# Optimization experiments

Hardware: AMD Instinct MI355X
Metric: run time of the kernel (lower is better)

Reference implementation:

```python
import jax, jax.numpy as jnp
import numpy as np

B, H, C_LEN, Q_LEN = 64, 128, 1024, 128


def setup_inputs() -> dict:
    key = jax.random.key(0)
    k1, k2, k3 = jax.random.split(key, 3)
    context = jax.random.normal(k1, (B, H, C_LEN), dtype=jnp.float32)
    question = jax.random.normal(k2, (B, H, Q_LEN), dtype=jnp.float32)
    lim = np.sqrt(1.0 / H)
    w = jax.random.uniform(k3, (3 * H,), dtype=jnp.float32, minval=-lim, maxval=lim)
    return {"context": context, "question": question, "w": w}


def reference(context, question, w):
    # context: (B, H, C), question: (B, H, Q); w: (3H,) with cat order (q, c, cq)
    h = w.shape[0] // 3
    w_q, w_c, w_cq = w[:h], w[h:2 * h], w[2 * h:]
    c = jnp.transpose(context, (0, 2, 1))   # (B, C, H)
    q = jnp.transpose(question, (0, 2, 1))  # (B, Q, H)
    # trilinear similarity s[b,i,j] = c_i.w_c + q_j.w_q + (c_i*w_cq).q_j  -> (B, C, Q)
    s = (c @ w_c)[:, :, None] + (q @ w_q)[:, None, :] \
        + jnp.einsum('bih,bjh->bij', c * w_cq, q)
    # original applies softmax over dim=1 (context axis) for BOTH s1 and s2
    s1 = jax.nn.softmax(s, axis=1)           # (B, C, Q)
    a = jnp.einsum('bij,bjh->bih', s1, q)    # (B, C, H)
    l = jnp.einsum('bij,bkj->bik', s1, s1)   # (B, C, C)
    b = jnp.einsum('bik,bkh->bih', l, c)     # (B, C, H)
    out = jnp.concatenate([c, a, c * a, c * b], axis=2)  # (B, C, 4H)
    # dropout disabled (drop_prob=0) for deterministic reference
    return jnp.transpose(out, (0, 2, 1))     # (B, 4H, C)
```

## Files before the change

kernel.cpp:

```cpp
#include <hip/hip_runtime.h>

#define BB 64
#define HH 128
#define CC 1024
#define QQ 128

typedef unsigned short u16;
typedef unsigned int u32;
using bf16x8 = __attribute__((ext_vector_type(8))) short;
using f32x4 = __attribute__((ext_vector_type(4))) float;

#define MFMA16(a, b, c) __builtin_amdgcn_mfma_f32_16x16x32_bf16(a, b, c, 0, 0, 0)

__device__ __forceinline__ u16 f2b(float f) {
  union { float f; u32 i; } v; v.f = f;
  u32 r = v.i + 0x7FFFu + ((v.i >> 16) & 1u);
  return (u16)(r >> 16);
}
__device__ __forceinline__ u32 pack_hi2(float a, float b) {
  return (__float_as_uint(a) >> 16) | (__float_as_uint(b) & 0xFFFF0000u);
}
__device__ __forceinline__ u32 pack_lo2(float a, float b) {
  float ra = a - __uint_as_float(__float_as_uint(a) & 0xFFFF0000u);
  float rb = b - __uint_as_float(__float_as_uint(b) & 0xFFFF0000u);
  return (__float_as_uint(ra) >> 16) | (__float_as_uint(rb) & 0xFFFF0000u);
}

__device__ __forceinline__ void stage16(const float* __restrict__ p,
                                        u16* dhi, u16* dlo) {
  float4 a0 = *(const float4*)p;
  float4 a1 = *(const float4*)(p + 4);
  float4 a2 = *(const float4*)(p + 8);
  float4 a3 = *(const float4*)(p + 12);
  uint4 h0 = {pack_hi2(a0.x, a0.y), pack_hi2(a0.z, a0.w),
              pack_hi2(a1.x, a1.y), pack_hi2(a1.z, a1.w)};
  uint4 h1 = {pack_hi2(a2.x, a2.y), pack_hi2(a2.z, a2.w),
              pack_hi2(a3.x, a3.y), pack_hi2(a3.z, a3.w)};
  uint4 l0 = {pack_lo2(a0.x, a0.y), pack_lo2(a0.z, a0.w),
              pack_lo2(a1.x, a1.y), pack_lo2(a1.z, a1.w)};
  uint4 l1 = {pack_lo2(a2.x, a2.y), pack_lo2(a2.z, a2.w),
              pack_lo2(a3.x, a3.y), pack_lo2(a3.z, a3.w)};
  *(uint4*)dhi = h0;
  *(uint4*)(dhi + 8) = h1;
  *(uint4*)dlo = l0;
  *(uint4*)(dlo + 8) = l1;
}

__global__ __launch_bounds__(256) void k_qw(
    const float* __restrict__ qst, const float* __restrict__ w,
    u16* __restrict__ qwh, u16* __restrict__ qwl) {
  const int b = blockIdx.x;
  const int tid = threadIdx.x;
  __shared__ float ld[128 * 129];
  __shared__ float wcq[128];
  const float* qb = qst + (size_t)b * HH * QQ;
#pragma unroll
  for (int rep = 0; rep < 16; ++rep) {
    int h = rep * 8 + (tid >> 5);
    int jo = (tid & 31) * 4;
    float4 v = *(const float4*)(qb + (size_t)h * QQ + jo);
    float* d = &ld[h * 129 + jo];
    d[0] = v.x; d[1] = v.y; d[2] = v.z; d[3] = v.w;
  }
  if (tid < 128) wcq[tid] = w[2 * HH + tid];
  __syncthreads();
  const int j = tid >> 1;
  const int hh0 = (tid & 1) * 64;
  u16* oh = qwh + (size_t)b * 144 * 128 + j * 128 + hh0;
  u16* ol = qwl + (size_t)b * 144 * 128 + j * 128 + hh0;
#pragma unroll
  for (int g = 0; g < 8; ++g) {
    u32 hw[4], lw[4];
#pragma unroll
    for (int p = 0; p < 4; ++p) {
      int h = hh0 + g * 8 + p * 2;
      float a = ld[h * 129 + j] * wcq[h];
      float c = ld[(h + 1) * 129 + j] * wcq[h + 1];
      hw[p] = pack_hi2(a, c);
      lw[p] = pack_lo2(a, c);
    }
    uint4 vh = {hw[0], hw[1], hw[2], hw[3]};
    uint4 vl = {lw[0], lw[1], lw[2], lw[3]};
    *(uint4*)(oh + g * 8) = vh;
    *(uint4*)(ol + g * 8) = vl;
  }
  if (tid < 128) {
    int jr = 128 + (tid >> 3);
    int hc = (tid & 7) * 16;
    u32 hw[8], lw[8];
#pragma unroll
    for (int p = 0; p < 8; ++p) { hw[p] = 0; lw[p] = 0; }
    if (jr == 128) {
#pragma unroll
      for (int p = 0; p < 8; ++p) {
        float a = w[HH + hc + p * 2];
        float c = w[HH + hc + p * 2 + 1];
        hw[p] = pack_hi2(a, c);
        lw[p] = pack_lo2(a, c);
      }
    }
    u16* ph = qwh + (size_t)b * 144 * 128 + (size_t)jr * 128 + hc;
    u16* pl = qwl + (size_t)b * 144 * 128 + (size_t)jr * 128 + hc;
    uint4 vh0 = {hw[0], hw[1], hw[2], hw[3]};
    uint4 vh1 = {hw[4], hw[5], hw[6], hw[7]};
    uint4 vl0 = {lw[0], lw[1], lw[2], lw[3]};
    uint4 vl1 = {lw[4], lw[5], lw[6], lw[7]};
    *(uint4*)ph = vh0; *(uint4*)(ph + 8) = vh1;
    *(uint4*)pl = vl0; *(uint4*)(pl + 8) = vl1;
  }
}

__global__ __launch_bounds__(256) void k_ct(
    const float* __restrict__ ctx, u16* __restrict__ cTh) {
  const int b = blockIdx.x;
  const int i0 = blockIdx.y * 128;
  const int tid = threadIdx.x;
  __shared__ float ld[128 * 129];
  const float* cb = ctx + (size_t)b * HH * CC;
#pragma unroll
  for (int rep = 0; rep < 16; ++rep) {
    int h = rep * 8 + (tid >> 5);
    int io = (tid & 31) * 4;
    float4 v = *(const float4*)(cb + (size_t)h * CC + i0 + io);
    float* d = &ld[h * 129 + io];
    d[0] = v.x; d[1] = v.y; d[2] = v.z; d[3] = v.w;
  }
  __syncthreads();
  const int i = tid >> 1;
  const int hh0 = (tid & 1) * 64;
  u16* oh = cTh + (size_t)b * CC * HH + (size_t)(i0 + i) * 128 + hh0;
#pragma unroll
  for (int g = 0; g < 8; ++g) {
    u32 hw[4];
#pragma unroll
    for (int p = 0; p < 4; ++p) {
      int h = hh0 + g * 8 + p * 2;
      hw[p] = pack_hi2(ld[h * 129 + i], ld[(h + 1) * 129 + i]);
    }
    uint4 vh = {hw[0], hw[1], hw[2], hw[3]};
    *(uint4*)(oh + g * 8) = vh;
  }
}

__global__ __launch_bounds__(512) void k0_softmax(
    const u16* __restrict__ cTh, const u16* __restrict__ qwh,
    const u16* __restrict__ qwl, u16* __restrict__ s1ws,
    u16* __restrict__ s1tb) {
  const int b = blockIdx.x;
  const int j0 = blockIdx.y * 16;
  const int tid = threadIdx.x;
  const int lane = tid & 63;
  const int wv = tid >> 6;
  const int l15 = lane & 15, l4 = lane >> 4;
  __shared__ float wred[2][8][4][4];

  const u16* cb = cTh + (size_t)b * CC * HH;
  const u16* qhp = qwh + (size_t)b * 144 * 128;
  const u16* qlp = qwl + (size_t)b * 144 * 128;

  bf16x8 aqh[4], aql[4], axh[4];
#pragma unroll
  for (int kk = 0; kk < 4; ++kk) {
    const int off = kk * 32 + l4 * 8;
    aqh[kk] = *(const bf16x8*)(qhp + (size_t)(j0 + l15) * 128 + off);
    aql[kk] = *(const bf16x8*)(qlp + (size_t)(j0 + l15) * 128 + off);
    axh[kk] = *(const bf16x8*)(qhp + (size_t)(128 + l15) * 128 + off);
  }

  f32x4 sv[8];
  float cwcv[8];
#pragma unroll
  for (int it = 0; it < 8; ++it) {
    const int i = wv * 128 + it * 16 + l15;
    f32x4 aR = {0.f, 0.f, 0.f, 0.f};
    f32x4 aX = {0.f, 0.f, 0.f, 0.f};
#pragma unroll
    for (int kk = 0; kk < 4; ++kk) {
      bf16x8 bh = *(const bf16x8*)(cb + (size_t)i * 128 + kk * 32 + l4 * 8);
      aR = MFMA16(aqh[kk], bh, aR);
      aR = MFMA16(aql[kk], bh, aR);
      aX = MFMA16(axh[kk], bh, aX);
    }
    cwcv[it] = __shfl(aX[0], l15);
    sv[it] = aR;
  }
#pragma unroll
  for (int it = 0; it < 8; ++it)
#pragma unroll
    for (int r = 0; r < 4; ++r) sv[it][r] += cwcv[it];

  float mj[4];
#pragma unroll
  for (int r = 0; r < 4; ++r) {
    float m = sv[0][r];
#pragma unroll
    for (int it = 1; it < 8; ++it) m = fmaxf(m, sv[it][r]);
#pragma unroll
    for (int msk = 1; msk < 16; msk <<= 1) m = fmaxf(m, __shfl_xor(m, msk));
    mj[r] = m;
  }
  if (l15 == 0) {
#pragma unroll
    for (int r = 0; r < 4; ++r) wred[0][wv][l4][r] = mj[r];
  }
  __syncthreads();
  float gm[4];
#pragma unroll
  for (int r = 0; r < 4; ++r) {
    float m = wred[0][0][l4][r];
#pragma unroll
    for (int w2 = 1; w2 < 8; ++w2) m = fmaxf(m, wred[0][w2][l4][r]);
    gm[r] = m;
  }

#pragma unroll
  for (int it = 0; it < 8; ++it)
#pragma unroll
    for (int r = 0; r < 4; ++r) sv[it][r] = __expf(sv[it][r] - gm[r]);
  float sj[4];
#pragma unroll
  for (int r = 0; r < 4; ++r) {
    float s = 0.f;
#pragma unroll
    for (int it = 0; it < 8; ++it) s += sv[it][r];
#pragma unroll
    for (int msk = 1; msk < 16; msk <<= 1) s += __shfl_xor(s, msk);
    sj[r] = s;
  }
  if (l15 == 0) {
#pragma unroll
    for (int r = 0; r < 4; ++r) wred[1][wv][l4][r] = sj[r];
  }
  __syncthreads();
  float inv_[4];
#pragma unroll
  for (int r = 0; r < 4; ++r) {
    float s = 0.f;
#pragma unroll
    for (int w2 = 0; w2 < 8; ++w2) s += wred[1][w2][l4][r];
    inv_[r] = 1.0f / s;
  }

  u16* ws = s1ws + (size_t)b * QQ * CC;
  u16* tb = s1tb + (size_t)b * (16 * 1024 * 8);
#pragma unroll
  for (int it = 0; it < 8; ++it) {
    const int i = wv * 128 + it * 16 + l15;
#pragma unroll
    for (int r = 0; r < 4; ++r) {
      const int j = j0 + l4 * 4 + r;
      u16 pv = f2b(sv[it][r] * inv_[r]);
      ws[(size_t)j * CC + i] = pv;
      tb[((size_t)(j >> 3) * 1024 + i) * 8 + (j & 7)] = pv;
    }
  }
}

__global__ __launch_bounds__(256) void k2_t(
    const float* __restrict__ ctx, const u16* __restrict__ s1ws,
    float* __restrict__ tT) {
  const int b = blockIdx.x;
  const int h0 = (blockIdx.y >> 1) * 32;
  const int j0 = (blockIdx.y & 1) * 64;
  const int tid = threadIdx.x;
  const int lane = tid & 63;
  const int wv = tid >> 6;
  const int l15 = lane & 15, l4 = lane >> 4;

  __shared__ u16 sHi[32 * 136];
  __shared__ u16 sLo[32 * 136];

  f32x4 acc[2];
  acc[0] = 0.f; acc[1] = 0.f;

  const float* cb = ctx + ((size_t)b * HH + h0) * CC;
  const u16* sb = s1ws + ((size_t)b * QQ + j0 + wv * 16 + l15) * CC;
  const int srow = tid >> 3;
  const int scol = (tid & 7) * 16;

  for (int k0 = 0; k0 < CC; k0 += 128) {
    __syncthreads();
    stage16(cb + (size_t)srow * CC + k0 + scol,
            &sHi[srow * 136 + scol], &sLo[srow * 136 + scol]);
    __syncthreads();
#pragma unroll
    for (int kk = 0; kk < 4; ++kk) {
      bf16x8 bf = *(const bf16x8*)(sb + k0 + kk * 32 + l4 * 8);
#pragma unroll
      for (int ht = 0; ht < 2; ++ht) {
        const int ar = (ht * 16 + l15) * 136 + kk * 32 + l4 * 8;
        bf16x8 ah = *(const bf16x8*)&sHi[ar];
        bf16x8 al = *(const bf16x8*)&sLo[ar];
        acc[ht] = MFMA16(ah, bf, acc[ht]);
        acc[ht] = MFMA16(al, bf, acc[ht]);
      }
    }
  }
  float* tb = tT + (size_t)b * HH * QQ;
#pragma unroll
  for (int ht = 0; ht < 2; ++ht)
#pragma unroll
    for (int r = 0; r < 4; ++r)
      tb[(size_t)(h0 + ht * 16 + l4 * 4 + r) * QQ + j0 + wv * 16 + l15] =
          acc[ht][r];
}

__global__ __launch_bounds__(256, 2) void k3_out(
    const float* __restrict__ ctx, const float* __restrict__ qst,
    const u16* __restrict__ s1tb, const float* __restrict__ tT,
    float* __restrict__ out) {
  const int b = blockIdx.x;
  const int i0 = blockIdx.y * 128;
  const int tid = threadIdx.x;
  const int lane = tid & 63;
  const int wv = tid >> 6;
  const int l15 = lane & 15, l4 = lane >> 4;

  __shared__ u16 qHi[128 * 40], qLo[128 * 40];
  __shared__ u16 tHi[128 * 40], tLo[128 * 40];

  f32x4 accA[8][2], accB[8][2];
#pragma unroll
  for (int it = 0; it < 8; ++it)
#pragma unroll
    for (int ht = 0; ht < 2; ++ht) { accA[it][ht] = 0.f; accB[it][ht] = 0.f; }

  const u16* stb = s1tb + (size_t)b * (16 * 1024 * 8);
  const float* qb = qst + (size_t)b * HH * QQ;
  const float* tb = tT + (size_t)b * HH * QQ;
  const int srow = tid >> 1;
  const int scol = (tid & 1) * 16;

  for (int ks = 0; ks < 4; ++ks) {
    const int jb = ks * 32;
    __syncthreads();
    stage16(qb + (size_t)srow * QQ + jb + scol,
            &qHi[srow * 40 + scol], &qLo[srow * 40 + scol]);
    stage16(tb + (size_t)srow * QQ + jb + scol,
            &tHi[srow * 40 + scol], &tLo[srow * 40 + scol]);
    __syncthreads();
    bf16x8 qh[2], ql[2], th[2], tl[2];
#pragma unroll
    for (int ht = 0; ht < 2; ++ht) {
      const int ar = (wv * 32 + ht * 16 + l15) * 40 + l4 * 8;
      qh[ht] = *(const bf16x8*)&qHi[ar];
      ql[ht] = *(const bf16x8*)&qLo[ar];
      th[ht] = *(const bf16x8*)&tHi[ar];
      tl[ht] = *(const bf16x8*)&tLo[ar];
    }
#pragma unroll
    for (int half = 0; half < 2; ++half) {
      bf16x8 bfr[4];
#pragma unroll
      for (int t4 = 0; t4 < 4; ++t4) {
        const int it = half * 4 + t4;
        bfr[t4] = *(const bf16x8*)(stb +
            ((size_t)(ks * 4 + l4) * 1024 + i0 + it * 16 + l15) * 8);
      }
#pragma unroll
      for (int t4 = 0; t4 < 4; ++t4) {
        const int it = half * 4 + t4;
#pragma unroll
        for (int ht = 0; ht < 2; ++ht) {
          accA[it][ht] = MFMA16(qh[ht], bfr[t4], accA[it][ht]);
          accA[it][ht] = MFMA16(ql[ht], bfr[t4], accA[it][ht]);
          accB[it][ht] = MFMA16(th[ht], bfr[t4], accB[it][ht]);
          accB[it][ht] = MFMA16(tl[ht], bfr[t4], accB[it][ht]);
        }
      }
    }
  }

  const float* cb = ctx + (size_t)b * HH * CC;
  float* ob = out + (size_t)b * 4 * HH * CC;
#pragma unroll
  for (int it = 0; it < 8; ++it) {
    const int ii = i0 + it * 16 + l15;
#pragma unroll
    for (int ht = 0; ht < 2; ++ht) {
#pragma unroll
      for (int r = 0; r < 4; ++r) {
        const int h = wv * 32 + ht * 16 + l4 * 4 + r;
        const size_t base = (size_t)h * CC + ii;
        const float cv = cb[base];
        const float av = accA[it][ht][r];
        const float bv = accB[it][ht][r];
        ob[base] = cv;
        ob[(size_t)HH * CC + base] = av;
        ob[(size_t)2 * HH * CC + base] = cv * av;
        ob[(size_t)3 * HH * CC + base] = cv * bv;
      }
    }
  }
}

extern "C" void kernel_launch(void* const* d_in, const int* in_sizes, int n_in,
                              void* d_out, int out_size, void* d_ws, size_t ws_size,
                              hipStream_t stream) {
  const float* ctx = (const float*)d_in[0];
  const float* qst = (const float*)d_in[1];
  const float* w = (const float*)d_in[2];
  for (int k = 0; k < n_in; ++k) {
    if (in_sizes[k] == BB * HH * CC) ctx = (const float*)d_in[k];
    else if (in_sizes[k] == BB * HH * QQ) qst = (const float*)d_in[k];
    else if (in_sizes[k] == 3 * HH) w = (const float*)d_in[k];
  }
  float* out = (float*)d_out;

  u16* s1ws = (u16*)d_ws;
  u16* s1tb = (u16*)((char*)d_ws + (size_t)16 * 1024 * 1024);
  float* tT = (float*)((char*)d_ws + (size_t)32 * 1024 * 1024);

  char* ob = (char*)d_out;
  u16* qwl = (u16*)(ob + 112721920);
  u16* qwh = (u16*)(ob + 115081216);
  u16* cTh = (u16*)(ob + 117440512);

  k_qw<<<BB, 256, 0, stream>>>(qst, w, qwh, qwl);
  k_ct<<<dim3(BB, 8), 256, 0, stream>>>(ctx, cTh);
  k0_softmax<<<dim3(BB, 8), 512, 0, stream>>>(cTh, qwh, qwl, s1ws, s1tb);
  k2_t<<<dim3(BB, 8), 256, 0, stream>>>(ctx, s1ws, tT);
  k3_out<<<dim3(BB, 8), 256, 0, stream>>>(ctx, qst, s1tb, tT, out);
}
```

Before: 245.7 us.

## Fuse prep kernels and fold context-by-softmax product into softmax kernel

Merges the question-weight and context-transpose prep kernels into one launch with an extra grid row. Folds the k2_t reduction (context times s1 over the context axis) into the softmax kernel: the normalized s1 tile is kept in LDS and each wave reads the context rows straight from global memory, splitting them into hi/lo bf16 for MFMA. This removes the s1ws global round-trip and two launches. In exchange, every softmax block now re-reads the full per-batch context (8x redundant across j-blocks), and there is a larger LDS footprint.

Result: no change. 248.9 us, median of 2 (+1.3%).

```diff
diff --git a/kernel.cpp b/kernel.cpp
--- a/kernel.cpp
+++ b/kernel.cpp
@@ -46,106 +46,105 @@
   *(uint4*)(dlo + 8) = l1;
 }
 
-__global__ __launch_bounds__(256) void k_qw(
-    const float* __restrict__ qst, const float* __restrict__ w,
+__global__ __launch_bounds__(256) void k_prep(
+    const float* __restrict__ ctx, const float* __restrict__ qst,
+    const float* __restrict__ w, u16* __restrict__ cTh,
     u16* __restrict__ qwh, u16* __restrict__ qwl) {
   const int b = blockIdx.x;
+  const int y = blockIdx.y;
   const int tid = threadIdx.x;
   __shared__ float ld[128 * 129];
   __shared__ float wcq[128];
-  const float* qb = qst + (size_t)b * HH * QQ;
-#pragma unroll
-  for (int rep = 0; rep < 16; ++rep) {
-    int h = rep * 8 + (tid >> 5);
-    int jo = (tid & 31) * 4;
-    float4 v = *(const float4*)(qb + (size_t)h * QQ + jo);
-    float* d = &ld[h * 129 + jo];
-    d[0] = v.x; d[1] = v.y; d[2] = v.z; d[3] = v.w;
-  }
-  if (tid < 128) wcq[tid] = w[2 * HH + tid];
-  __syncthreads();
-  const int j = tid >> 1;
-  const int hh0 = (tid & 1) * 64;
-  u16* oh = qwh + (size_t)b * 144 * 128 + j * 128 + hh0;
-  u16* ol = qwl + (size_t)b * 144 * 128 + j * 128 + hh0;
-#pragma unroll
-  for (int g = 0; g < 8; ++g) {
-    u32 hw[4], lw[4];
-#pragma unroll
-    for (int p = 0; p < 4; ++p) {
-      int h = hh0 + g * 8 + p * 2;
-      float a = ld[h * 129 + j] * wcq[h];
-      float c = ld[(h + 1) * 129 + j] * wcq[h + 1];
-      hw[p] = pack_hi2(a, c);
-      lw[p] = pack_lo2(a, c);
-    }
-    uint4 vh = {hw[0], hw[1], hw[2], hw[3]};
-    uint4 vl = {lw[0], lw[1], lw[2], lw[3]};
-    *(uint4*)(oh + g * 8) = vh;
-    *(uint4*)(ol + g * 8) = vl;
-  }
-  if (tid < 128) {
-    int jr = 128 + (tid >> 3);
-    int hc = (tid & 7) * 16;
-    u32 hw[8], lw[8];
-#pragma unroll
-    for (int p = 0; p < 8; ++p) { hw[p] = 0; lw[p] = 0; }
-    if (jr == 128) {
-#pragma unroll
-      for (int p = 0; p < 8; ++p) {
-        float a = w[HH + hc + p * 2];
-        float c = w[HH + hc + p * 2 + 1];
+
+  if (y < 8) {
+    const int i0 = y * 128;
+    const float* cb = ctx + (size_t)b * HH * CC;
+#pragma unroll
+    for (int rep = 0; rep < 16; ++rep) {
+      int h = rep * 8 + (tid >> 5);
+      int io = (tid & 31) * 4;
+      float4 v = *(const float4*)(cb + (size_t)h * CC + i0 + io);
+      float* d = &ld[h * 129 + io];
+      d[0] = v.x; d[1] = v.y; d[2] = v.z; d[3] = v.w;
+    }
+    __syncthreads();
+    const int i = tid >> 1;
+    const int hh0 = (tid & 1) * 64;
+    u16* oh = cTh + (size_t)b * CC * HH + (size_t)(i0 + i) * 128 + hh0;
+#pragma unroll
+    for (int g = 0; g < 8; ++g) {
+      u32 hw[4];
+#pragma unroll
+      for (int p = 0; p < 4; ++p) {
+        int h = hh0 + g * 8 + p * 2;
+        hw[p] = pack_hi2(ld[h * 129 + i], ld[(h + 1) * 129 + i]);
+      }
+      uint4 vh = {hw[0], hw[1], hw[2], hw[3]};
+      *(uint4*)(oh + g * 8) = vh;
+    }
+  } else {
+    const float* qb = qst + (size_t)b * HH * QQ;
+#pragma unroll
+    for (int rep = 0; rep < 16; ++rep) {
+      int h = rep * 8 + (tid >> 5);
+      int jo = (tid & 31) * 4;
+      float4 v = *(const float4*)(qb + (size_t)h * QQ + jo);
+      float* d = &ld[h * 129 + jo];
+      d[0] = v.x; d[1] = v.y; d[2] = v.z; d[3] = v.w;
+    }
+    if (tid < 128) wcq[tid] = w[2 * HH + tid];
+    __syncthreads();
+    const int j = tid >> 1;
+    const int hh0 = (tid & 1) * 64;
+    u16* oh = qwh + (size_t)b * 144 * 128 + j * 128 + hh0;
+    u16* ol = qwl + (size_t)b * 144 * 128 + j * 128 + hh0;
+#pragma unroll
+    for (int g = 0; g < 8; ++g) {
+      u32 hw[4], lw[4];
+#pragma unroll
+      for (int p = 0; p < 4; ++p) {
+        int h = hh0 + g * 8 + p * 2;
+        float a = ld[h * 129 + j] * wcq[h];
+        float c = ld[(h + 1) * 129 + j] * wcq[h + 1];
         hw[p] = pack_hi2(a, c);
         lw[p] = pack_lo2(a, c);
       }
-    }
-    u16* ph = qwh + (size_t)b * 144 * 128 + (size_t)jr * 128 + hc;
-    u16* pl = qwl + (size_t)b * 144 * 128 + (size_t)jr * 128 + hc;
-    uint4 vh0 = {hw[0], hw[1], hw[2], hw[3]};
-    uint4 vh1 = {hw[4], hw[5], hw[6], hw[7]};
-    uint4 vl0 = {lw[0], lw[1], lw[2], lw[3]};
-    uint4 vl1 = {lw[4], lw[5], lw[6], lw[7]};
-    *(uint4*)ph = vh0; *(uint4*)(ph + 8) = vh1;
-    *(uint4*)pl = vl0; *(uint4*)(pl + 8) = vl1;
-  }
-}
-
-__global__ __launch_bounds__(256) void k_ct(
-    const float* __restrict__ ctx, u16* __restrict__ cTh) {
-  const int b = blockIdx.x;
-  const int i0 = blockIdx.y * 128;
-  const int tid = threadIdx.x;
-  __shared__ float ld[128 * 129];
-  const float* cb = ctx + (size_t)b * HH * CC;
-#pragma unroll
-  for (int rep = 0; rep < 16; ++rep) {
-    int h = rep * 8 + (tid >> 5);
-    int io = (tid & 31) * 4;
-    float4 v = *(const float4*)(cb + (size_t)h * CC + i0 + io);
-    float* d = &ld[h * 129 + io];
-    d[0] = v.x; d[1] = v.y; d[2] = v.z; d[3] = v.w;
-  }
-  __syncthreads();
-  const int i = tid >> 1;
-  const int hh0 = (tid & 1) * 64;
-  u16* oh = cTh + (size_t)b * CC * HH + (size_t)(i0 + i) * 128 + hh0;
-#pragma unroll
-  for (int g = 0; g < 8; ++g) {
-    u32 hw[4];
-#pragma unroll
-    for (int p = 0; p < 4; ++p) {
-      int h = hh0 + g * 8 + p * 2;
-      hw[p] = pack_hi2(ld[h * 129 + i], ld[(h + 1) * 129 + i]);
-    }
-    uint4 vh = {hw[0], hw[1], hw[2], hw[3]};
-    *(uint4*)(oh + g * 8) = vh;
-  }
-}
-
-__global__ __launch_bounds__(512) void k0_softmax(
-    const u16* __restrict__ cTh, const u16* __restrict__ qwh,
-    const u16* __restrict__ qwl, u16* __restrict__ s1ws,
-    u16* __restrict__ s1tb) {
+      uint4 vh = {hw[0], hw[1], hw[2], hw[3]};
+      uint4 vl = {lw[0], lw[1], lw[2], lw[3]};
+      *(uint4*)(oh + g * 8) = vh;
+      *(uint4*)(ol + g * 8) = vl;
+    }
+    if (tid < 128) {
+      int jr = 128 + (tid >> 3);
+      int hc = (tid & 7) * 16;
+      u32 hw[8], lw[8];
+#pragma unroll
+      for (int p = 0; p < 8; ++p) { hw[p] = 0; lw[p] = 0; }
+      if (jr == 128) {
+#pragma unroll
+        for (int p = 0; p < 8; ++p) {
+          float a = w[HH + hc + p * 2];
+          float c = w[HH + hc + p * 2 + 1];
+          hw[p] = pack_hi2(a, c);
+          lw[p] = pack_lo2(a, c);
+        }
+      }
+      u16* ph = qwh + (size_t)b * 144 * 128 + (size_t)jr * 128 + hc;
+      u16* pl = qwl + (size_t)b * 144 * 128 + (size_t)jr * 128 + hc;
+      uint4 vh0 = {hw[0], hw[1], hw[2], hw[3]};
+      uint4 vh1 = {hw[4], hw[5], hw[6], hw[7]};
+      uint4 vl0 = {lw[0], lw[1], lw[2], lw[3]};
+      uint4 vl1 = {lw[4], lw[5], lw[6], lw[7]};
+      *(uint4*)ph = vh0; *(uint4*)(ph + 8) = vh1;
+      *(uint4*)pl = vl0; *(uint4*)(pl + 8) = vl1;
+    }
+  }
+}
+
+__global__ __launch_bounds__(512) void k0_fused(
+    const float* __restrict__ ctx, const u16* __restrict__ cTh,
+    const u16* __restrict__ qwh, const u16* __restrict__ qwl,
+    u16* __restrict__ s1tb, float* __restrict__ tT) {
   const int b = blockIdx.x;
   const int j0 = blockIdx.y * 16;
   const int tid = threadIdx.x;
@@ -153,6 +152,7 @@
   const int wv = tid >> 6;
   const int l15 = lane & 15, l4 = lane >> 4;
   __shared__ float wred[2][8][4][4];
+  __shared__ u16 s1l[16 * 1026];
 
   const u16* cb = cTh + (size_t)b * CC * HH;
   const u16* qhp = qwh + (size_t)b * 144 * 128;
@@ -241,7 +241,6 @@
     inv_[r] = 1.0f / s;
   }
 
-  u16* ws = s1ws + (size_t)b * QQ * CC;
   u16* tb = s1tb + (size_t)b * (16 * 1024 * 8);
 #pragma unroll
   for (int it = 0; it < 8; ++it) {
@@ -250,59 +249,30 @@
     for (int r = 0; r < 4; ++r) {
       const int j = j0 + l4 * 4 + r;
       u16 pv = f2b(sv[it][r] * inv_[r]);
-      ws[(size_t)j * CC + i] = pv;
       tb[((size_t)(j >> 3) * 1024 + i) * 8 + (j & 7)] = pv;
-    }
-  }
-}
-
-__global__ __launch_bounds__(256) void k2_t(
-    const float* __restrict__ ctx, const u16* __restrict__ s1ws,
-    float* __restrict__ tT) {
-  const int b = blockIdx.x;
-  const int h0 = (blockIdx.y >> 1) * 32;
-  const int j0 = (blockIdx.y & 1) * 64;
-  const int tid = threadIdx.x;
-  const int lane = tid & 63;
-  const int wv = tid >> 6;
-  const int l15 = lane & 15, l4 = lane >> 4;
-
-  __shared__ u16 sHi[32 * 136];
-  __shared__ u16 sLo[32 * 136];
-
-  f32x4 acc[2];
-  acc[0] = 0.f; acc[1] = 0.f;
-
-  const float* cb = ctx + ((size_t)b * HH + h0) * CC;
-  const u16* sb = s1ws + ((size_t)b * QQ + j0 + wv * 16 + l15) * CC;
-  const int srow = tid >> 3;
-  const int scol = (tid & 7) * 16;
-
-  for (int k0 = 0; k0 < CC; k0 += 128) {
-    __syncthreads();
-    stage16(cb + (size_t)srow * CC + k0 + scol,
-            &sHi[srow * 136 + scol], &sLo[srow * 136 + scol]);
-    __syncthreads();
-#pragma unroll
-    for (int kk = 0; kk < 4; ++kk) {
-      bf16x8 bf = *(const bf16x8*)(sb + k0 + kk * 32 + l4 * 8);
-#pragma unroll
-      for (int ht = 0; ht < 2; ++ht) {
-        const int ar = (ht * 16 + l15) * 136 + kk * 32 + l4 * 8;
-        bf16x8 ah = *(const bf16x8*)&sHi[ar];
-        bf16x8 al = *(const bf16x8*)&sLo[ar];
-        acc[ht] = MFMA16(ah, bf, acc[ht]);
-        acc[ht] = MFMA16(al, bf, acc[ht]);
-      }
-    }
-  }
-  float* tb = tT + (size_t)b * HH * QQ;
-#pragma unroll
-  for (int ht = 0; ht < 2; ++ht)
-#pragma unroll
-    for (int r = 0; r < 4; ++r)
-      tb[(size_t)(h0 + ht * 16 + l4 * 4 + r) * QQ + j0 + wv * 16 + l15] =
-          acc[ht][r];
+      s1l[(l4 * 4 + r) * 1026 + i] = pv;
+    }
+  }
+  __syncthreads();
+
+  const float* cxr = ctx + ((size_t)b * HH + wv * 16 + l15) * CC;
+  f32x4 tacc = {0.f, 0.f, 0.f, 0.f};
+#pragma unroll 4
+  for (int kk = 0; kk < 32; ++kk) {
+    const int ib = kk * 32 + l4 * 8;
+    float4 c0 = *(const float4*)(cxr + ib);
+    float4 c1 = *(const float4*)(cxr + ib + 4);
+    uint4 hb = {pack_hi2(c0.x, c0.y), pack_hi2(c0.z, c0.w),
+                pack_hi2(c1.x, c1.y), pack_hi2(c1.z, c1.w)};
+    uint4 lb = {pack_lo2(c0.x, c0.y), pack_lo2(c0.z, c0.w),
+                pack_lo2(c1.x, c1.y), pack_lo2(c1.z, c1.w)};
+    bf16x8 af = *(const bf16x8*)&s1l[l15 * 1026 + ib];
+    tacc = MFMA16(af, *(const bf16x8*)&hb, tacc);
+    tacc = MFMA16(af, *(const bf16x8*)&lb, tacc);
+  }
+  float* tw = tT + (size_t)b * HH * QQ + (size_t)(wv * 16 + l15) * QQ + j0;
+#pragma unroll
+  for (int r = 0; r < 4; ++r) tw[l4 * 4 + r] = tacc[r];
 }
 
 __global__ __launch_bounds__(256, 2) void k3_out(
@@ -407,18 +377,15 @@
   }
   float* out = (float*)d_out;
 
-  u16* s1ws = (u16*)d_ws;
-  u16* s1tb = (u16*)((char*)d_ws + (size_t)16 * 1024 * 1024);
-  float* tT = (float*)((char*)d_ws + (size_t)32 * 1024 * 1024);
+  u16* s1tb = (u16*)d_ws;
+  float* tT = (float*)((char*)d_ws + (size_t)16 * 1024 * 1024);
 
   char* ob = (char*)d_out;
   u16* qwl = (u16*)(ob + 112721920);
   u16* qwh = (u16*)(ob + 115081216);
   u16* cTh = (u16*)(ob + 117440512);
 
-  k_qw<<<BB, 256, 0, stream>>>(qst, w, qwh, qwl);
-  k_ct<<<dim3(BB, 8), 256, 0, stream>>>(ctx, cTh);
-  k0_softmax<<<dim3(BB, 8), 512, 0, stream>>>(cTh, qwh, qwl, s1ws, s1tb);
-  k2_t<<<dim3(BB, 8), 256, 0, stream>>>(ctx, s1ws, tT);
+  k_prep<<<dim3(BB, 9), 256, 0, stream>>>(ctx, qst, w, cTh, qwh, qwl);
+  k0_fused<<<dim3(BB, 8), 512, 0, stream>>>(ctx, cTh, qwh, qwl, s1tb, tT);
   k3_out<<<dim3(BB, 8), 256, 0, stream>>>(ctx, qst, s1tb, tT, out);
 }
```
